# Kernel optimization log

Hardware: AMD Instinct MI355X
Metric: run time of the kernel (lower is better)

## Reference

```python
import jax, jax.numpy as jnp
import numpy as np

DIM = 1024
H = 16
HEAD_DIM = 64
HIDDEN = H * HEAD_DIM  # == DIM, required by the module's reshape
SCALE = HEAD_DIM ** -0.5


def setup_inputs() -> dict:
    key = jax.random.key(0)
    k_x, k_qkv, k_w1, k_b1 = jax.random.split(key, 4)
    B, N = 8, 1024
    x = jax.random.normal(k_x, (B, N, DIM), dtype=jnp.float32)
    # nn.Linear stores weight as [out, in]; we keep [in, out] for x @ W
    w_qkv = jax.random.normal(k_qkv, (DIM, 3 * HIDDEN), dtype=jnp.float32) * (DIM ** -0.5)
    w_out = jax.random.normal(k_w1, (HIDDEN, DIM), dtype=jnp.float32) * (HIDDEN ** -0.5)
    b_out = jax.random.normal(k_b1, (DIM,), dtype=jnp.float32) * 0.02
    return {"x": x, "w_qkv": w_qkv, "w_out": w_out, "b_out": b_out}


def reference(x, w_qkv, w_out, b_out):
    B, N, C = x.shape
    # QKV projection (no bias), split into heads
    qkv = (x @ w_qkv).reshape(B, N, 3, H, C // H)
    q, k, v = qkv[:, :, 0], qkv[:, :, 1], qkv[:, :, 2]  # [B, N, H, d]
    attn = jnp.einsum("bqhd,bkhd->bhqk", q, k) * SCALE
    attn = jax.nn.softmax(attn, axis=-1)  # dropout inactive at eval
    out = jnp.einsum("bhqk,bkhd->bqhd", attn, v).reshape(B, N, C)
    return out @ w_out + b_out
```

## Files before the change

### kernel.cpp

```cpp
#include <hip/hip_runtime.h>
#include <hip/hip_bf16.h>

#define B_SZ 8
#define SEQ 1024
#define DIM_ 1024
#define NH 16
#define HD 64
#define M_TOT (B_SZ*SEQ)
#define N_QKV (3*DIM_)

typedef __attribute__((ext_vector_type(8))) short bf16x8;
typedef __attribute__((ext_vector_type(4))) float f32x4;

typedef const __attribute__((address_space(1))) void gvoid;
typedef __attribute__((address_space(3))) void lvoid;

__device__ __forceinline__ short f2bf(float f){
  union { __hip_bfloat16 h; short s; } u;
  u.h = __float2bfloat16(f);
  return u.s;
}

__global__ void cvt_kernel(const float* __restrict__ in, short* __restrict__ out, int n4){
  int i = blockIdx.x*blockDim.x + threadIdx.x;
  int stride = gridDim.x*blockDim.x;
  for (; i < n4; i += stride){
    float4 v = reinterpret_cast<const float4*>(in)[i];
    short4 s;
    s.x = f2bf(v.x); s.y = f2bf(v.y); s.z = f2bf(v.z); s.w = f2bf(v.w);
    reinterpret_cast<short4*>(out)[i] = s;
  }
}

__global__ void tconv_kernel(const float* __restrict__ in, short* __restrict__ out, int R, int C){
  __shared__ alignas(16) short tile[64][66];
  const int l = threadIdx.x & 63, w = threadIdx.x >> 6;
  const int r0 = blockIdx.y * 64, c0 = blockIdx.x * 64;
  #pragma unroll
  for (int rr = 0; rr < 16; ++rr){
    int r = w + rr*4;
    tile[r][l] = f2bf(in[(size_t)(r0+r)*C + c0 + l]);
  }
  __syncthreads();
  #pragma unroll
  for (int cc = 0; cc < 16; ++cc){
    int c = w + cc*4;
    out[(size_t)(c0+c)*R + r0 + l] = tile[l][c];
  }
}

template<int EPI, int GX, int NOFF>
__global__ __launch_bounds__(256, 4) void gemm5(
    const short* __restrict__ A, const short* __restrict__ Bt,
    int M, int Nn, int K,
    short* __restrict__ Qb, short* __restrict__ Kb, short* __restrict__ Vtb,
    const float* __restrict__ bias, float* __restrict__ outF)
{
  __shared__ alignas(16) short As[2][128*32];
  __shared__ alignas(16) short Bs[2][128*32];

  const int orig = blockIdx.x;
  const int xcd = orig & 7, t = orig >> 3;
  const int by = xcd*8 + t/GX, bx = t % GX;

  const int tid = threadIdx.x;
  const int l = tid & 63, wid = tid >> 6;
  const int wr = wid >> 1, wc = wid & 1;
  const int lr = l & 15, lw = l >> 4;
  const int sw = (lr >> 1) & 3;
  const int m0 = by * 128, n0 = (bx + NOFF) * 128;

  f32x4 acc[4][4];
  const f32x4 zz = {0.f,0.f,0.f,0.f};
  #pragma unroll
  for (int m=0;m<4;m++)
    #pragma unroll
    for (int n=0;n<4;n++) acc[m][n] = zz;

  auto STAGE = [&](int buf, int kt){
    const int k0 = kt << 5;
    #pragma unroll
    for (int j=0;j<2;j++){
      const int idx = j*256 + tid;
      const int row = idx >> 2;
      const int ws  = (idx & 3) ^ ((row >> 1) & 3);
      __builtin_amdgcn_global_load_lds(
          (gvoid*)(A + (size_t)(m0+row)*K + k0 + ws*8),
          (lvoid*)(&As[buf][idx*8]), 16, 0, 0);
    }
    #pragma unroll
    for (int j=0;j<2;j++){
      const int idx = j*256 + tid;
      const int row = idx >> 2;
      const int ws  = (idx & 3) ^ ((row >> 1) & 3);
      __builtin_amdgcn_global_load_lds(
          (gvoid*)(Bt + (size_t)(n0+row)*K + k0 + ws*8),
          (lvoid*)(&Bs[buf][idx*8]), 16, 0, 0);
    }
  };

  STAGE(0, 0);
  __syncthreads();

  const int NT = K >> 5;
  int buf = 0;
  for (int kt = 0; kt < NT; ++kt){
    if (kt + 1 < NT) STAGE(buf ^ 1, kt + 1);

    bf16x8 af[4], bfr[4];
    const int wsel = (lw ^ sw) << 3;
    #pragma unroll
    for (int m=0;m<4;m++){
      const int r = wr*64 + m*16 + lr;
      af[m] = *(const bf16x8*)(&As[buf][r*32 + wsel]);
    }
    #pragma unroll
    for (int n=0;n<4;n++){
      const int r = wc*64 + n*16 + lr;
      bfr[n] = *(const bf16x8*)(&Bs[buf][r*32 + wsel]);
    }
    #pragma unroll
    for (int m=0;m<4;m++)
      #pragma unroll
      for (int n=0;n<4;n++)
        acc[m][n] = __builtin_amdgcn_mfma_f32_16x16x32_bf16(af[m], bfr[n], acc[m][n], 0, 0, 0);

    __syncthreads();
    buf ^= 1;
  }

  #pragma unroll
  for (int n=0;n<4;n++){
    const int col = n0 + wc*64 + n*16 + lr;
    if (EPI == 0){
      const int three = col >> 10;
      const int cc = col & 1023;
      const int h = cc >> 6, d = cc & 63;
      #pragma unroll
      for (int m=0;m<4;m++){
        const int rbase = m0 + wr*64 + m*16 + (lw<<2);
        const int b = rbase >> 10, nn = rbase & 1023;
        const int bh = b*NH + h;
        if (three == 2){
          short4 pk;
          pk.x = f2bf(acc[m][n][0]); pk.y = f2bf(acc[m][n][1]);
          pk.z = f2bf(acc[m][n][2]); pk.w = f2bf(acc[m][n][3]);
          *(short4*)(&Vtb[((size_t)bh*HD + d)*SEQ + nn]) = pk;
        } else if (three == 0){
          #pragma unroll
          for (int ri=0;ri<4;ri++)
            Qb[((size_t)bh*SEQ + nn + ri)*HD + d] = f2bf(acc[m][n][ri] * 0.1803368801f);
        } else {
          #pragma unroll
          for (int ri=0;ri<4;ri++)
            Kb[((size_t)bh*SEQ + nn + ri)*HD + d] = f2bf(acc[m][n][ri]);
        }
      }
    } else {
      const float bv = bias[col];
      #pragma unroll
      for (int m=0;m<4;m++){
        const int rbase = m0 + wr*64 + m*16 + (lw<<2);
        #pragma unroll
        for (int ri=0;ri<4;ri++)
          outF[(size_t)(rbase+ri)*Nn + col] = acc[m][n][ri] + bv;
      }
    }
  }
}

__global__ __launch_bounds__(256) void attn_kernel(
    const short* __restrict__ Q, const short* __restrict__ Kb,
    const short* __restrict__ Vt, short* __restrict__ Ao)
{
  __shared__ alignas(16) short Ks[2][64*64];
  __shared__ alignas(16) short Vs[2][64*64];
  __shared__ alignas(16) short Ps[4][32*72];

  const int tid = threadIdx.x;
  const int l = tid & 63, w = tid >> 6;
  const int orig = blockIdx.x;
  const int xcd = orig & 7, n_ = orig >> 3;
  const int g = n_ >> 3, qt = n_ & 7;
  const int bh = g*8 + xcd;
  const int b = bh >> 4, h = bh & 15;
  const size_t base = (size_t)bh << 16;

  const int lr = l & 15;
  const int q4 = l >> 4;
  const int lk = q4 << 3;
  const int sw8 = lr & 7;

  const int qrowA = qt*128 + w*32 + lr;
  const short* qpA = Q + base + (size_t)qrowA*HD + lk;
  const bf16x8 qfA0 = *(const bf16x8*)qpA;
  const bf16x8 qfA1 = *(const bf16x8*)(qpA + 32);
  const short* qpB = qpA + 16*HD;
  const bf16x8 qfB0 = *(const bf16x8*)qpB;
  const bf16x8 qfB1 = *(const bf16x8*)(qpB + 32);

  float lA = 0.f, lB = 0.f;
  f32x4 oA[4], oB[4];
  #pragma unroll
  for (int i=0;i<4;i++){ oA[i] = f32x4{0.f,0.f,0.f,0.f}; oB[i] = f32x4{0.f,0.f,0.f,0.f}; }

  bf16x8 kr[2], vr[2];
  auto load_tile = [&](int kt){
    const int kv0 = kt*64;
    #pragma unroll
    for (int p=0;p<2;p++){
      const int idx = tid + p*256;
      const int row = idx >> 3, c8 = (idx & 7) << 3;
      kr[p] = *(const bf16x8*)(Kb + base + (size_t)(kv0+row)*HD + c8);
      vr[p] = *(const bf16x8*)(Vt + base + (size_t)row*SEQ + kv0 + c8);
    }
  };
  auto write_tile = [&](int bi){
    #pragma unroll
    for (int p=0;p<2;p++){
      const int idx = tid + p*256;
      const int row = idx >> 3;
      const int wsw = ((idx & 7) ^ (row & 7)) << 3;
      *(bf16x8*)(&Ks[bi][row*64 + wsw]) = kr[p];
      *(bf16x8*)(&Vs[bi][row*64 + wsw]) = vr[p];
    }
  };

  load_tile(0);
  write_tile(0);
  __syncthreads();

  int cur = 0;
  for (int kt = 0; kt < 16; ++kt){
    if (kt < 15) load_tile(kt+1);

    const short* kb = &Ks[cur][0];
    const short* vb = &Vs[cur][0];

    f32x4 sA[4], sB[4];
    #pragma unroll
    for (int cg=0;cg<4;cg++){ sA[cg] = f32x4{0.f,0.f,0.f,0.f}; sB[cg] = f32x4{0.f,0.f,0.f,0.f}; }
    __builtin_amdgcn_s_setprio(1);
    #pragma unroll
    for (int cg=0;cg<4;cg++){
      const short* kp = kb + (cg*16 + lr)*64;
      bf16x8 kf0 = *(const bf16x8*)(kp + ((q4     ^ sw8) << 3));
      bf16x8 kf1 = *(const bf16x8*)(kp + (((q4+4) ^ sw8) << 3));
      sA[cg] = __builtin_amdgcn_mfma_f32_16x16x32_bf16(kf0, qfA0, sA[cg], 0,0,0);
      sA[cg] = __builtin_amdgcn_mfma_f32_16x16x32_bf16(kf1, qfA1, sA[cg], 0,0,0);
      sB[cg] = __builtin_amdgcn_mfma_f32_16x16x32_bf16(kf0, qfB0, sB[cg], 0,0,0);
      sB[cg] = __builtin_amdgcn_mfma_f32_16x16x32_bf16(kf1, qfB1, sB[cg], 0,0,0);
    }
    __builtin_amdgcn_s_setprio(0);

    short* pw = &Ps[w][0];
    float rsA = 0.f, rsB = 0.f;
    #pragma unroll
    for (int cg=0;cg<4;cg++){
      float a0 = __builtin_amdgcn_exp2f(sA[cg][0]);
      float a1 = __builtin_amdgcn_exp2f(sA[cg][1]);
      float a2 = __builtin_amdgcn_exp2f(sA[cg][2]);
      float a3 = __builtin_amdgcn_exp2f(sA[cg][3]);
      rsA += (a0+a1)+(a2+a3);
      short4 ka; ka.x=f2bf(a0); ka.y=f2bf(a1); ka.z=f2bf(a2); ka.w=f2bf(a3);
      *(short4*)(pw + lr*72 + cg*16 + q4*4) = ka;
      float b0 = __builtin_amdgcn_exp2f(sB[cg][0]);
      float b1 = __builtin_amdgcn_exp2f(sB[cg][1]);
      float b2 = __builtin_amdgcn_exp2f(sB[cg][2]);
      float b3 = __builtin_amdgcn_exp2f(sB[cg][3]);
      rsB += (b0+b1)+(b2+b3);
      short4 kb_; kb_.x=f2bf(b0); kb_.y=f2bf(b1); kb_.z=f2bf(b2); kb_.w=f2bf(b3);
      *(short4*)(pw + (16+lr)*72 + cg*16 + q4*4) = kb_;
    }
    rsA += __shfl_xor(rsA, 16); rsA += __shfl_xor(rsA, 32); lA += rsA;
    rsB += __shfl_xor(rsB, 16); rsB += __shfl_xor(rsB, 32); lB += rsB;

    const bf16x8 paA0 = *(const bf16x8*)(pw + lr*72 + lk);
    const bf16x8 paA1 = *(const bf16x8*)(pw + lr*72 + lk + 32);
    const bf16x8 paB0 = *(const bf16x8*)(pw + (16+lr)*72 + lk);
    const bf16x8 paB1 = *(const bf16x8*)(pw + (16+lr)*72 + lk + 32);

    __builtin_amdgcn_s_setprio(1);
    #pragma unroll
    for (int dg=0;dg<4;dg++){
      const short* vp = vb + (dg*16 + lr)*64;
      bf16x8 vf0 = *(const bf16x8*)(vp + ((q4     ^ sw8) << 3));
      bf16x8 vf1 = *(const bf16x8*)(vp + (((q4+4) ^ sw8) << 3));
      oA[dg] = __builtin_amdgcn_mfma_f32_16x16x32_bf16(paA0, vf0, oA[dg], 0,0,0);
      oA[dg] = __builtin_amdgcn_mfma_f32_16x16x32_bf16(paA1, vf1, oA[dg], 0,0,0);
      oB[dg] = __builtin_amdgcn_mfma_f32_16x16x32_bf16(paB0, vf0, oB[dg], 0,0,0);
      oB[dg] = __builtin_amdgcn_mfma_f32_16x16x32_bf16(paB1, vf1, oB[dg], 0,0,0);
    }
    __builtin_amdgcn_s_setprio(0);

    if (kt < 15) write_tile(cur ^ 1);
    __syncthreads();
    cur ^= 1;
  }

  float linvA[4], linvB[4];
  #pragma unroll
  for (int ri=0;ri<4;ri++){
    linvA[ri] = 1.0f / __shfl(lA, (q4<<2) + ri);
    linvB[ri] = 1.0f / __shfl(lB, (q4<<2) + ri);
  }
  #pragma unroll
  for (int ri=0;ri<4;ri++){
    const int rowA = qt*128 + w*32 + (q4<<2) + ri;
    short* opA = Ao + ((size_t)(b*SEQ + rowA))*DIM_ + h*HD;
    short* opB = opA + 16*DIM_;
    #pragma unroll
    for (int dg=0;dg<4;dg++){
      opA[dg*16 + lr] = f2bf(oA[dg][ri] * linvA[ri]);
      opB[dg*16 + lr] = f2bf(oB[dg][ri] * linvB[ri]);
    }
  }
}

extern "C" void kernel_launch(void* const* d_in, const int* in_sizes, int n_in,
                              void* d_out, int out_size, void* d_ws, size_t ws_size,
                              hipStream_t stream)
{
  (void)in_sizes; (void)n_in; (void)out_size; (void)ws_size;
  const float* x     = (const float*)d_in[0];
  const float* w_qkv = (const float*)d_in[1];
  const float* w_out = (const float*)d_in[2];
  const float* b_out = (const float*)d_in[3];
  float* out = (float*)d_out;

  char* ws = (char*)d_ws;
  const size_t MB = (size_t)1 << 20;
  short* xb    = (short*)(ws);
  short* wqkvT = (short*)(ws + 16*MB);
  short* woutT = (short*)(ws + 22*MB);
  short* Qb    = (short*)(ws + 24*MB);
  short* Kb    = (short*)(ws + 40*MB);
  short* Vtb   = (short*)(ws + 56*MB);
  short* Aob   = (short*)(ws + 72*MB);

  cvt_kernel<<<2048, 256, 0, stream>>>(x, xb, (M_TOT*DIM_)/4);
  tconv_kernel<<<dim3(N_QKV/64, DIM_/64), 256, 0, stream>>>(w_qkv, wqkvT, DIM_, N_QKV);
  tconv_kernel<<<dim3(DIM_/64, DIM_/64), 256, 0, stream>>>(w_out, woutT, DIM_, DIM_);

  gemm5<0,24,0><<<1536, 256, 0, stream>>>(
      xb, wqkvT, M_TOT, N_QKV, DIM_, Qb, Kb, Vtb, nullptr, nullptr);

  attn_kernel<<<1024, 256, 0, stream>>>(Qb, Kb, Vtb, Aob);

  gemm5<1,8,0><<<512, 256, 0, stream>>>(
      Aob, woutT, M_TOT, DIM_, DIM_, nullptr, nullptr, nullptr, b_out, out);
}
```

Before: 167.5 us.

## Triple-buffer GEMM LDS staging with explicit vmcnt waits and barriers

Converts the bf16 GEMM's double-buffered global-to-LDS pipeline into a three-stage ring. Loads now run two k-tiles ahead, and partial s_waitcnt vmcnt counts replace the full __syncthreads, so more memory latency can be hidden behind the MFMA work. The cost is 50% more LDS per block and a lower occupancy bound in launch_bounds (3 instead of 4), plus two barriers per iteration. The hand-written wait counts must match the four loads issued per stage.

```diff
diff --git a/kernel.cpp b/kernel.cpp
--- a/kernel.cpp
+++ b/kernel.cpp
@@ -50,18 +50,18 @@
 }
 
 template<int EPI, int GX, int NOFF>
-__global__ __launch_bounds__(256, 4) void gemm5(
+__global__ __launch_bounds__(256, 3) void gemm7(
     const short* __restrict__ A, const short* __restrict__ Bt,
     int M, int Nn, int K,
     short* __restrict__ Qb, short* __restrict__ Kb, short* __restrict__ Vtb,
     const float* __restrict__ bias, float* __restrict__ outF)
 {
-  __shared__ alignas(16) short As[2][128*32];
-  __shared__ alignas(16) short Bs[2][128*32];
+  __shared__ alignas(16) short As[3][128*32];
+  __shared__ alignas(16) short Bs[3][128*32];
 
   const int orig = blockIdx.x;
-  const int xcd = orig & 7, t = orig >> 3;
-  const int by = xcd*8 + t/GX, bx = t % GX;
+  const int xcd = orig & 7, t0_ = orig >> 3;
+  const int by = xcd*8 + t0_/GX, bx = t0_ % GX;
 
   const int tid = threadIdx.x;
   const int l = tid & 63, wid = tid >> 6;
@@ -77,7 +77,7 @@
     #pragma unroll
     for (int n=0;n<4;n++) acc[m][n] = zz;
 
-  auto STAGE = [&](int buf, int kt){
+  auto STAGE = [&](int q, int kt){
     const int k0 = kt << 5;
     #pragma unroll
     for (int j=0;j<2;j++){
@@ -86,7 +86,7 @@
       const int ws  = (idx & 3) ^ ((row >> 1) & 3);
       __builtin_amdgcn_global_load_lds(
           (gvoid*)(A + (size_t)(m0+row)*K + k0 + ws*8),
-          (lvoid*)(&As[buf][idx*8]), 16, 0, 0);
+          (lvoid*)(&As[q][idx*8]), 16, 0, 0);
     }
     #pragma unroll
     for (int j=0;j<2;j++){
@@ -95,29 +95,45 @@
       const int ws  = (idx & 3) ^ ((row >> 1) & 3);
       __builtin_amdgcn_global_load_lds(
           (gvoid*)(Bt + (size_t)(n0+row)*K + k0 + ws*8),
-          (lvoid*)(&Bs[buf][idx*8]), 16, 0, 0);
+          (lvoid*)(&Bs[q][idx*8]), 16, 0, 0);
     }
   };
 
   STAGE(0, 0);
-  __syncthreads();
+  STAGE(1, 1);
+  asm volatile("s_waitcnt vmcnt(4)" ::: "memory");
+  __builtin_amdgcn_sched_barrier(0);
+  __builtin_amdgcn_s_barrier();
+  __builtin_amdgcn_sched_barrier(0);
 
   const int NT = K >> 5;
-  int buf = 0;
-  for (int kt = 0; kt < NT; ++kt){
-    if (kt + 1 < NT) STAGE(buf ^ 1, kt + 1);
+  int cur = 0, sb = 2;
+  for (int t = 0; t < NT; ++t){
+    if (t + 2 < NT){
+      STAGE(sb, t+2);
+      asm volatile("s_waitcnt vmcnt(8)" ::: "memory");
+    } else if (t + 1 < NT){
+      asm volatile("s_waitcnt vmcnt(4)" ::: "memory");
+    } else {
+      asm volatile("s_waitcnt vmcnt(0)" ::: "memory");
+    }
+    __builtin_amdgcn_sched_barrier(0);
+    __builtin_amdgcn_s_barrier();
+    __builtin_amdgcn_sched_barrier(0);
 
     bf16x8 af[4], bfr[4];
     const int wsel = (lw ^ sw) << 3;
+    const short* ab = &As[cur][0];
+    const short* bb = &Bs[cur][0];
     #pragma unroll
     for (int m=0;m<4;m++){
       const int r = wr*64 + m*16 + lr;
-      af[m] = *(const bf16x8*)(&As[buf][r*32 + wsel]);
+      af[m] = *(const bf16x8*)(ab + r*32 + wsel);
     }
     #pragma unroll
     for (int n=0;n<4;n++){
       const int r = wc*64 + n*16 + lr;
-      bfr[n] = *(const bf16x8*)(&Bs[buf][r*32 + wsel]);
+      bfr[n] = *(const bf16x8*)(bb + r*32 + wsel);
     }
     #pragma unroll
     for (int m=0;m<4;m++)
@@ -125,8 +141,13 @@
       for (int n=0;n<4;n++)
         acc[m][n] = __builtin_amdgcn_mfma_f32_16x16x32_bf16(af[m], bfr[n], acc[m][n], 0, 0, 0);
 
-    __syncthreads();
-    buf ^= 1;
+    asm volatile("s_waitcnt lgkmcnt(0)" ::: "memory");
+    __builtin_amdgcn_sched_barrier(0);
+    __builtin_amdgcn_s_barrier();
+    __builtin_amdgcn_sched_barrier(0);
+
+    cur = (cur==2) ? 0 : cur+1;
+    sb  = (sb ==2) ? 0 : sb +1;
   }
 
   #pragma unroll
@@ -342,11 +363,11 @@
   tconv_kernel<<<dim3(N_QKV/64, DIM_/64), 256, 0, stream>>>(w_qkv, wqkvT, DIM_, N_QKV);
   tconv_kernel<<<dim3(DIM_/64, DIM_/64), 256, 0, stream>>>(w_out, woutT, DIM_, DIM_);
 
-  gemm5<0,24,0><<<1536, 256, 0, stream>>>(
+  gemm7<0,24,0><<<1536, 256, 0, stream>>>(
       xb, wqkvT, M_TOT, N_QKV, DIM_, Qb, Kb, Vtb, nullptr, nullptr);
 
   attn_kernel<<<1024, 256, 0, stream>>>(Qb, Kb, Vtb, Aob);
 
-  gemm5<1,8,0><<<512, 256, 0, stream>>>(
+  gemm7<1,8,0><<<512, 256, 0, stream>>>(
       Aob, woutT, M_TOT, DIM_, DIM_, nullptr, nullptr, nullptr, b_out, out);
 }
```

Measured after the change: 167.4 us (median of 2 runs). No clear change (-0.1%).

## Fuse fp32-to-bf16 input conversion into QKV GEMM operand loading

Applied to the files above, without the earlier changes.

Removes the standalone conversion kernel for x and has the QKV GEMM stage fp32 tiles of x directly into LDS (with an XOR swizzle), converting to bf16 in registers before each MFMA. This eliminates a full write and re-read of a bf16 copy of the activations and one kernel launch. In exchange the GEMM reads twice as many bytes per A tile, repeats the conversion for every column block, uses more LDS and lowers the occupancy hint to 3 blocks per CU. The out-projection GEMM is simplified to a bias-only epilogue template.

```diff
diff --git a/kernel.cpp b/kernel.cpp
--- a/kernel.cpp
+++ b/kernel.cpp
@@ -21,17 +21,6 @@
   return u.s;
 }
 
-__global__ void cvt_kernel(const float* __restrict__ in, short* __restrict__ out, int n4){
-  int i = blockIdx.x*blockDim.x + threadIdx.x;
-  int stride = gridDim.x*blockDim.x;
-  for (; i < n4; i += stride){
-    float4 v = reinterpret_cast<const float4*>(in)[i];
-    short4 s;
-    s.x = f2bf(v.x); s.y = f2bf(v.y); s.z = f2bf(v.z); s.w = f2bf(v.w);
-    reinterpret_cast<short4*>(out)[i] = s;
-  }
-}
-
 __global__ void tconv_kernel(const float* __restrict__ in, short* __restrict__ out, int R, int C){
   __shared__ alignas(16) short tile[64][66];
   const int l = threadIdx.x & 63, w = threadIdx.x >> 6;
@@ -49,11 +38,10 @@
   }
 }
 
-template<int EPI, int GX, int NOFF>
+template<int GX>
 __global__ __launch_bounds__(256, 4) void gemm5(
     const short* __restrict__ A, const short* __restrict__ Bt,
     int M, int Nn, int K,
-    short* __restrict__ Qb, short* __restrict__ Kb, short* __restrict__ Vtb,
     const float* __restrict__ bias, float* __restrict__ outF)
 {
   __shared__ alignas(16) short As[2][128*32];
@@ -68,7 +56,7 @@
   const int wr = wid >> 1, wc = wid & 1;
   const int lr = l & 15, lw = l >> 4;
   const int sw = (lr >> 1) & 3;
-  const int m0 = by * 128, n0 = (bx + NOFF) * 128;
+  const int m0 = by * 128, n0 = bx * 128;
 
   f32x4 acc[4][4];
   const f32x4 zz = {0.f,0.f,0.f,0.f};
@@ -132,38 +120,129 @@
   #pragma unroll
   for (int n=0;n<4;n++){
     const int col = n0 + wc*64 + n*16 + lr;
-    if (EPI == 0){
-      const int three = col >> 10;
-      const int cc = col & 1023;
-      const int h = cc >> 6, d = cc & 63;
+    const float bv = bias[col];
+    #pragma unroll
+    for (int m=0;m<4;m++){
+      const int rbase = m0 + wr*64 + m*16 + (lw<<2);
       #pragma unroll
-      for (int m=0;m<4;m++){
-        const int rbase = m0 + wr*64 + m*16 + (lw<<2);
-        const int b = rbase >> 10, nn = rbase & 1023;
-        const int bh = b*NH + h;
-        if (three == 2){
-          short4 pk;
-          pk.x = f2bf(acc[m][n][0]); pk.y = f2bf(acc[m][n][1]);
-          pk.z = f2bf(acc[m][n][2]); pk.w = f2bf(acc[m][n][3]);
-          *(short4*)(&Vtb[((size_t)bh*HD + d)*SEQ + nn]) = pk;
-        } else if (three == 0){
-          #pragma unroll
-          for (int ri=0;ri<4;ri++)
-            Qb[((size_t)bh*SEQ + nn + ri)*HD + d] = f2bf(acc[m][n][ri] * 0.1803368801f);
-        } else {
-          #pragma unroll
-          for (int ri=0;ri<4;ri++)
-            Kb[((size_t)bh*SEQ + nn + ri)*HD + d] = f2bf(acc[m][n][ri]);
-        }
-      }
-    } else {
-      const float bv = bias[col];
+      for (int ri=0;ri<4;ri++)
+        outF[(size_t)(rbase+ri)*Nn + col] = acc[m][n][ri] + bv;
+    }
+  }
+}
+
+template<int GX>
+__global__ __launch_bounds__(256, 3) void gemm6(
+    const float* __restrict__ A, const short* __restrict__ Bt,
+    int M, int Nn, int K,
+    short* __restrict__ Qb, short* __restrict__ Kb, short* __restrict__ Vtb)
+{
+  __shared__ alignas(16) float Af[2][128*32];
+  __shared__ alignas(16) short Bs[2][128*32];
+
+  const int orig = blockIdx.x;
+  const int xcd = orig & 7, t = orig >> 3;
+  const int by = xcd*8 + t/GX, bx = t % GX;
+
+  const int tid = threadIdx.x;
+  const int l = tid & 63, wid = tid >> 6;
+  const int wr = wid >> 1, wc = wid & 1;
+  const int lr = l & 15, lw = l >> 4;
+  const int swb = (lr >> 1) & 3;
+  const int swa = lr & 7;
+  const int m0 = by * 128, n0 = bx * 128;
+
+  f32x4 acc[4][4];
+  const f32x4 zz = {0.f,0.f,0.f,0.f};
+  #pragma unroll
+  for (int m=0;m<4;m++)
+    #pragma unroll
+    for (int n=0;n<4;n++) acc[m][n] = zz;
+
+  auto STAGE = [&](int buf, int kt){
+    const int k0 = kt << 5;
+    #pragma unroll
+    for (int j=0;j<4;j++){
+      const int idx = j*256 + tid;
+      const int row = idx >> 3;
+      const int ws  = (idx & 7) ^ (row & 7);
+      __builtin_amdgcn_global_load_lds(
+          (gvoid*)(A + (size_t)(m0+row)*K + k0 + ws*4),
+          (lvoid*)(&Af[buf][idx*4]), 16, 0, 0);
+    }
+    #pragma unroll
+    for (int j=0;j<2;j++){
+      const int idx = j*256 + tid;
+      const int row = idx >> 2;
+      const int ws  = (idx & 3) ^ ((row >> 1) & 3);
+      __builtin_amdgcn_global_load_lds(
+          (gvoid*)(Bt + (size_t)(n0+row)*K + k0 + ws*8),
+          (lvoid*)(&Bs[buf][idx*8]), 16, 0, 0);
+    }
+  };
+
+  STAGE(0, 0);
+  __syncthreads();
+
+  const int NT = K >> 5;
+  int buf = 0;
+  for (int kt = 0; kt < NT; ++kt){
+    if (kt + 1 < NT) STAGE(buf ^ 1, kt + 1);
+
+    bf16x8 af[4], bfr[4];
+    #pragma unroll
+    for (int m=0;m<4;m++){
+      const int r = wr*64 + m*16 + lr;
+      const float* ap = &Af[buf][r*32];
+      const int w0 = (2*lw)     ^ swa;
+      const int w1 = (2*lw + 1) ^ swa;
+      float4 fa = *(const float4*)(ap + w0*4);
+      float4 fb = *(const float4*)(ap + w1*4);
+      bf16x8 v;
+      v[0]=f2bf(fa.x); v[1]=f2bf(fa.y); v[2]=f2bf(fa.z); v[3]=f2bf(fa.w);
+      v[4]=f2bf(fb.x); v[5]=f2bf(fb.y); v[6]=f2bf(fb.z); v[7]=f2bf(fb.w);
+      af[m] = v;
+    }
+    const int wselb = (lw ^ swb) << 3;
+    #pragma unroll
+    for (int n=0;n<4;n++){
+      const int r = wc*64 + n*16 + lr;
+      bfr[n] = *(const bf16x8*)(&Bs[buf][r*32 + wselb]);
+    }
+    #pragma unroll
+    for (int m=0;m<4;m++)
       #pragma unroll
-      for (int m=0;m<4;m++){
-        const int rbase = m0 + wr*64 + m*16 + (lw<<2);
+      for (int n=0;n<4;n++)
+        acc[m][n] = __builtin_amdgcn_mfma_f32_16x16x32_bf16(af[m], bfr[n], acc[m][n], 0, 0, 0);
+
+    __syncthreads();
+    buf ^= 1;
+  }
+
+  #pragma unroll
+  for (int n=0;n<4;n++){
+    const int col = n0 + wc*64 + n*16 + lr;
+    const int three = col >> 10;
+    const int cc = col & 1023;
+    const int h = cc >> 6, d = cc & 63;
+    #pragma unroll
+    for (int m=0;m<4;m++){
+      const int rbase = m0 + wr*64 + m*16 + (lw<<2);
+      const int b = rbase >> 10, nn = rbase & 1023;
+      const int bh = b*NH + h;
+      if (three == 2){
+        short4 pk;
+        pk.x = f2bf(acc[m][n][0]); pk.y = f2bf(acc[m][n][1]);
+        pk.z = f2bf(acc[m][n][2]); pk.w = f2bf(acc[m][n][3]);
+        *(short4*)(&Vtb[((size_t)bh*HD + d)*SEQ + nn]) = pk;
+      } else if (three == 0){
         #pragma unroll
         for (int ri=0;ri<4;ri++)
-          outF[(size_t)(rbase+ri)*Nn + col] = acc[m][n][ri] + bv;
+          Qb[((size_t)bh*SEQ + nn + ri)*HD + d] = f2bf(acc[m][n][ri] * 0.1803368801f);
+      } else {
+        #pragma unroll
+        for (int ri=0;ri<4;ri++)
+          Kb[((size_t)bh*SEQ + nn + ri)*HD + d] = f2bf(acc[m][n][ri]);
       }
     }
   }
@@ -330,7 +409,6 @@
 
   char* ws = (char*)d_ws;
   const size_t MB = (size_t)1 << 20;
-  short* xb    = (short*)(ws);
   short* wqkvT = (short*)(ws + 16*MB);
   short* woutT = (short*)(ws + 22*MB);
   short* Qb    = (short*)(ws + 24*MB);
@@ -338,15 +416,14 @@
   short* Vtb   = (short*)(ws + 56*MB);
   short* Aob   = (short*)(ws + 72*MB);
 
-  cvt_kernel<<<2048, 256, 0, stream>>>(x, xb, (M_TOT*DIM_)/4);
   tconv_kernel<<<dim3(N_QKV/64, DIM_/64), 256, 0, stream>>>(w_qkv, wqkvT, DIM_, N_QKV);
   tconv_kernel<<<dim3(DIM_/64, DIM_/64), 256, 0, stream>>>(w_out, woutT, DIM_, DIM_);
 
-  gemm5<0,24,0><<<1536, 256, 0, stream>>>(
-      xb, wqkvT, M_TOT, N_QKV, DIM_, Qb, Kb, Vtb, nullptr, nullptr);
+  gemm6<24><<<1536, 256, 0, stream>>>(
+      x, wqkvT, M_TOT, N_QKV, DIM_, Qb, Kb, Vtb);
 
   attn_kernel<<<1024, 256, 0, stream>>>(Qb, Kb, Vtb, Aob);
 
-  gemm5<1,8,0><<<512, 256, 0, stream>>>(
-      Aob, woutT, M_TOT, DIM_, DIM_, nullptr, nullptr, nullptr, b_out, out);
-}
+  gemm5<8><<<512, 256, 0, stream>>>(
+      Aob, woutT, M_TOT, DIM_, DIM_, b_out, out);
+}
```

Measured after the change: 169.0 us. Within noise of the previous version (+0.9%).
